# Optimization experiments

Measured on AMD Instinct MI355X. Metric: run time of the kernel, lower is better.

## Reference

```python
import jax, jax.numpy as jnp
import numpy as np

DIM = 1536
NHEADS = 24
HEAD_DIM = DIM // NHEADS
EPS = 1e-6


def rms_norm(x):
    # normalize over last dim, no learned weight
    ms = jnp.mean(x * x, axis=-1, keepdims=True)
    return x * jax.lax.rsqrt(ms + EPS)


def rope_non_neox(x, cos, sin):
    # x: [B, S, H, D]; cos/sin: [S, D] -> broadcast [1, S, 1, D]
    # non-neox (GPT-J / interleaved) style: pairs are (x0,x1),(x2,x3),...
    c = cos[None, :, None, :]
    s = sin[None, :, None, :]
    x1 = x[..., 0::2]
    x2 = x[..., 1::2]
    c1 = c[..., 0::2]
    s1 = s[..., 0::2]
    o1 = x1 * c1 - x2 * s1
    o2 = x2 * c1 + x1 * s1
    out = jnp.stack([o1, o2], axis=-1).reshape(x.shape)
    return out


def setup_inputs() -> dict:
    key = jax.random.key(0)
    k1, k2, k3, k4, k5 = jax.random.split(key, 5)
    B, S = 4, 4096
    x = jax.random.normal(k1, (B, S, DIM), dtype=jnp.float32)
    # rotary tables: build valid cos/sin from random angles (interleaved duplication)
    half = HEAD_DIM // 2
    inv_freq = 1.0 / (10000.0 ** (jnp.arange(0, half, dtype=jnp.float32) / half))
    t = jnp.arange(S, dtype=jnp.float32)
    freqs = jnp.outer(t, inv_freq)  # [S, D/2]
    cos = jnp.repeat(jnp.cos(freqs), 2, axis=-1)  # [S, D] interleaved
    sin = jnp.repeat(jnp.sin(freqs), 2, axis=-1)
    w_qkv = jax.random.normal(k2, (DIM, 3 * DIM), dtype=jnp.float32) * (DIM ** -0.5)
    b_qkv = jax.random.normal(k3, (3 * DIM,), dtype=jnp.float32) * 0.02
    return {"x": x, "cos": cos, "sin": sin, "w_qkv": w_qkv, "b_qkv": b_qkv}


def reference(x, cos, sin, w_qkv, b_qkv):
    B, S, _ = x.shape
    H, D = NHEADS, HEAD_DIM
    qkv = jnp.einsum('bsd,de->bse', x, w_qkv) + b_qkv  # [B,S,3*DIM]
    q, k, v = jnp.split(qkv, 3, axis=-1)
    q = q.reshape(B, S, H, D)
    k = k.reshape(B, S, H, D)
    v = v.reshape(B, S, H, D)
    q = rms_norm(q)
    k = rms_norm(k)
    q = rope_non_neox(q, cos, sin)
    k = rope_non_neox(k, cos, sin)
    # SDPA: [B,H,S,D]
    qh = q.transpose(0, 2, 1, 3)
    kh = k.transpose(0, 2, 1, 3)
    vh = v.transpose(0, 2, 1, 3)
    scale = D ** -0.5
    scores = jnp.einsum('bhqd,bhkd->bhqk', qh, kh) * scale
    attn = jax.nn.softmax(scores, axis=-1)
    out = jnp.einsum('bhqk,bhkd->bhqd', attn, vh)
    out = out.transpose(0, 2, 1, 3).reshape(B, S, H * D)
    return out
```

## Files before the change

### kernel.cpp

```cpp
#include <hip/hip_runtime.h>

#define DIM   1536
#define NQKV  4608
#define NH    24
#define HD    64
#define BATCH 4
#define SEQ   4096
#define ROWS  16384

typedef _Float16 f16x8 __attribute__((ext_vector_type(8)));
typedef float    f32x4 __attribute__((ext_vector_type(4)));

__device__ __forceinline__ void gload_lds16(const void* g, void* l) {
  __builtin_amdgcn_global_load_lds(
      (const __attribute__((address_space(1))) unsigned int*)g,
      (__attribute__((address_space(3))) unsigned int*)l, 16, 0, 0);
}
__device__ __forceinline__ float fexp2(float x) {
#if __has_builtin(__builtin_amdgcn_exp2f)
  return __builtin_amdgcn_exp2f(x);
#else
  return exp2f(x);
#endif
}

#define QSCALE 0.18033688011112042f

__global__ __launch_bounds__(256) void convert_x(const float* __restrict__ X,
                                                 _Float16* __restrict__ Xh) {
  const int i = (blockIdx.x * 256 + threadIdx.x) * 8;
  float4 a = *(const float4*)(X + i);
  float4 b = *(const float4*)(X + i + 4);
  f16x8 h;
  h[0] = (_Float16)a.x; h[1] = (_Float16)a.y; h[2] = (_Float16)a.z; h[3] = (_Float16)a.w;
  h[4] = (_Float16)b.x; h[5] = (_Float16)b.y; h[6] = (_Float16)b.z; h[7] = (_Float16)b.w;
  *(f16x8*)(Xh + i) = h;
}

__global__ __launch_bounds__(256) void transpose_w(const float* __restrict__ W,
                                                   _Float16* __restrict__ Wt) {
  __shared__ float tile[32][33];
  const int tx = threadIdx.x, ty = threadIdx.y;
  const int k0 = blockIdx.y * 32, n0 = blockIdx.x * 32;
  #pragma unroll
  for (int i = 0; i < 32; i += 8)
    tile[ty + i][tx] = W[(size_t)(k0 + ty + i) * NQKV + n0 + tx];
  __syncthreads();
  #pragma unroll
  for (int i = 0; i < 32; i += 8)
    Wt[(size_t)(n0 + ty + i) * DIM + k0 + tx] = (_Float16)tile[tx][ty + i];
}

__global__ __launch_bounds__(256) void qkv_gemm(const _Float16* __restrict__ Xh,
                                                const _Float16* __restrict__ Wt,
                                                const float* __restrict__ Bias,
                                                _Float16* __restrict__ QKV) {
  __shared__ _Float16 As[128 * 64];
  __shared__ _Float16 Bs[128 * 64];
  const int w    = threadIdx.x >> 6;
  const int lane = threadIdx.x & 63;
  const int lr   = lane >> 3, lc = lane & 7;
  const int quad = lane >> 4, l15 = lane & 15;
  const int m0 = blockIdx.y * 128;
  const int n0 = blockIdx.x * 128;
  const int waveR = (w >> 1) * 64;
  const int waveC = (w & 1) * 64;

  f32x4 acc[4][4];
  #pragma unroll
  for (int i = 0; i < 4; i++)
    #pragma unroll
    for (int j = 0; j < 4; j++) acc[i][j] = (f32x4){0.f, 0.f, 0.f, 0.f};

  for (int kt = 0; kt < DIM / 64; ++kt) {
    const int k0 = kt * 64;
    #pragma unroll
    for (int i = 0; i < 4; ++i) {
      const int rr = w * 32 + i * 8;
      gload_lds16(Xh + (size_t)(m0 + rr + lr) * DIM + k0 + lc * 8, &As[rr * 64]);
      gload_lds16(Wt + (size_t)(n0 + rr + lr) * DIM + k0 + lc * 8, &Bs[rr * 64]);
    }
    __syncthreads();
    #pragma unroll
    for (int ks = 0; ks < 2; ++ks) {
      f16x8 aF[4], bF[4];
      #pragma unroll
      for (int t = 0; t < 4; t++)
        aF[t] = *(const f16x8*)&As[(waveR + t * 16 + l15) * 64 + ks * 32 + quad * 8];
      #pragma unroll
      for (int t = 0; t < 4; t++)
        bF[t] = *(const f16x8*)&Bs[(waveC + t * 16 + l15) * 64 + ks * 32 + quad * 8];
      #pragma unroll
      for (int mt = 0; mt < 4; mt++)
        #pragma unroll
        for (int nt = 0; nt < 4; nt++)
          acc[mt][nt] = __builtin_amdgcn_mfma_f32_16x16x32_f16(aF[mt], bF[nt], acc[mt][nt], 0, 0, 0);
    }
    __syncthreads();
  }
  #pragma unroll
  for (int nt = 0; nt < 4; nt++) {
    const int n = n0 + waveC + nt * 16 + l15;
    const float bias = Bias[n];
    #pragma unroll
    for (int mt = 0; mt < 4; mt++) {
      const int mBase = m0 + waveR + mt * 16 + quad * 4;
      #pragma unroll
      for (int r = 0; r < 4; r++)
        QKV[(size_t)(mBase + r) * NQKV + n] = (_Float16)(acc[mt][nt][r] + bias);
    }
  }
}

__global__ __launch_bounds__(256) void rms_rope(_Float16* __restrict__ QKV,
                                                const float* __restrict__ Cos,
                                                const float* __restrict__ Sin) {
  const int gw   = blockIdx.x * 4 + (threadIdx.x >> 6);
  const int lane = threadIdx.x & 63;
  const int row  = gw / NH;
  const int h    = gw - row * NH;
  const int s    = row & (SEQ - 1);

  _Float16* p = QKV + (size_t)row * NQKV + h * HD;
  float q = (float)p[lane];
  float k = (float)p[DIM + lane];

  float sq = q * q, sk = k * k;
  #pragma unroll
  for (int off = 1; off < 64; off <<= 1) {
    sq += __shfl_xor(sq, off);
    sk += __shfl_xor(sk, off);
  }
  q *= rsqrtf(sq * (1.f / 64.f) + 1e-6f);
  k *= rsqrtf(sk * (1.f / 64.f) + 1e-6f);

  const float c  = Cos[s * HD + lane];
  const float si = Sin[s * HD + lane];
  const float qp = __shfl_xor(q, 1);
  const float kp = __shfl_xor(k, 1);
  float oq, ok;
  if (lane & 1) { oq = q * c + qp * si; ok = k * c + kp * si; }
  else          { oq = q * c - qp * si; ok = k * c - kp * si; }

  p[lane]       = (_Float16)(oq * QSCALE);
  p[DIM + lane] = (_Float16)ok;
}

#define LSTR 72
__global__ __launch_bounds__(256) void flash_attn(const _Float16* __restrict__ QKV,
                                                  float* __restrict__ Out) {
  __shared__ __align__(16) _Float16 sm[2 * 64 * LSTR + 4 * 32 * LSTR];
  _Float16* Ks  = sm;
  _Float16* Vts = sm + 64 * LSTR;
  const int w = threadIdx.x >> 6;
  _Float16* Ps = sm + 2 * 64 * LSTR + w * 32 * LSTR;
  const int lane = threadIdx.x & 63;
  const int quad = lane >> 4, l15 = lane & 15;
  const int bh = blockIdx.y;
  const int qt = blockIdx.x;
  const int b  = bh / NH;
  const int h  = bh - b * NH;
  const size_t rowb = (size_t)b * SEQ * NQKV + (size_t)h * HD;

  f16x8 qreg[2][2];
  #pragma unroll
  for (int mt = 0; mt < 2; mt++)
    #pragma unroll
    for (int ks = 0; ks < 2; ks++) {
      const int row = qt * 128 + w * 32 + mt * 16 + l15;
      qreg[mt][ks] = *(const f16x8*)(QKV + rowb + (size_t)row * NQKV + ks * 32 + quad * 8);
    }

  f16x8 onesF;
  {
    const _Float16 one = (_Float16)(l15 == 0 ? 1.0f : 0.0f);
    #pragma unroll
    for (int j = 0; j < 8; j++) onesF[j] = one;
  }

  f32x4 o[2][4], o4[2];
  #pragma unroll
  for (int mt = 0; mt < 2; mt++) {
    o4[mt] = (f32x4){0.f, 0.f, 0.f, 0.f};
    #pragma unroll
    for (int t = 0; t < 4; t++) o[mt][t] = (f32x4){0.f, 0.f, 0.f, 0.f};
  }

  for (int kt = 0; kt < SEQ / 64; ++kt) {
    __syncthreads();
    #pragma unroll
    for (int i = 0; i < 2; i++) {
      const int chunk = threadIdx.x + i * 256;
      const int r = chunk >> 3, c0 = (chunk & 7) * 8;
      *(uint4*)&Ks[r * LSTR + c0] =
          *(const uint4*)(QKV + rowb + (size_t)(kt * 64 + r) * NQKV + DIM + c0);
    }
    #pragma unroll
    for (int i = 0; i < 2; i++) {
      const int c0 = w * 16 + i * 8;
      union { uint4 v; _Float16 u[8]; } d;
      d.v = *(const uint4*)(QKV + rowb + (size_t)(kt * 64 + lane) * NQKV + 2 * DIM + c0);
      #pragma unroll
      for (int j = 0; j < 8; j++) Vts[(c0 + j) * LSTR + lane] = d.u[j];
    }
    __syncthreads();

    f32x4 sacc[2][4];
    #pragma unroll
    for (int mt = 0; mt < 2; mt++)
      #pragma unroll
      for (int t = 0; t < 4; t++) sacc[mt][t] = (f32x4){0.f, 0.f, 0.f, 0.f};
    #pragma unroll
    for (int ks = 0; ks < 2; ks++) {
      f16x8 bF[4];
      #pragma unroll
      for (int t = 0; t < 4; t++)
        bF[t] = *(const f16x8*)&Ks[(t * 16 + l15) * LSTR + ks * 32 + quad * 8];
      #pragma unroll
      for (int mt = 0; mt < 2; mt++)
        #pragma unroll
        for (int t = 0; t < 4; t++)
          sacc[mt][t] = __builtin_amdgcn_mfma_f32_16x16x32_f16(qreg[mt][ks], bF[t], sacc[mt][t], 0, 0, 0);
    }

    #pragma unroll
    for (int mt = 0; mt < 2; mt++)
      #pragma unroll
      for (int t = 0; t < 4; t++)
        #pragma unroll
        for (int r = 0; r < 4; r++) {
          const _Float16 ph = (_Float16)fexp2(sacc[mt][t][r]);
          Ps[(mt * 16 + quad * 4 + r) * LSTR + t * 16 + l15] = ph;
        }

    #pragma unroll
    for (int ks = 0; ks < 2; ks++) {
      f16x8 pF[2];
      #pragma unroll
      for (int mt = 0; mt < 2; mt++)
        pF[mt] = *(const f16x8*)&Ps[(mt * 16 + l15) * LSTR + ks * 32 + quad * 8];
      #pragma unroll
      for (int t = 0; t < 4; t++) {
        f16x8 vF = *(const f16x8*)&Vts[(t * 16 + l15) * LSTR + ks * 32 + quad * 8];
        #pragma unroll
        for (int mt = 0; mt < 2; mt++)
          o[mt][t] = __builtin_amdgcn_mfma_f32_16x16x32_f16(pF[mt], vF, o[mt][t], 0, 0, 0);
      }
      #pragma unroll
      for (int mt = 0; mt < 2; mt++)
        o4[mt] = __builtin_amdgcn_mfma_f32_16x16x32_f16(pF[mt], onesF, o4[mt], 0, 0, 0);
    }
  }

  #pragma unroll
  for (int mt = 0; mt < 2; mt++) {
    float lrow[4];
    #pragma unroll
    for (int r = 0; r < 4; r++) lrow[r] = __shfl(o4[mt][r], lane & 48);
    #pragma unroll
    for (int t = 0; t < 4; t++)
      #pragma unroll
      for (int r = 0; r < 4; r++) {
        const int srow = qt * 128 + w * 32 + mt * 16 + quad * 4 + r;
        const int d = t * 16 + l15;
        Out[((size_t)(b * SEQ + srow)) * DIM + h * HD + d] = o[mt][t][r] / lrow[r];
      }
  }
}

extern "C" void kernel_launch(void* const* d_in, const int* in_sizes, int n_in,
                              void* d_out, int out_size, void* d_ws, size_t ws_size,
                              hipStream_t stream) {
  const float* X    = (const float*)d_in[0];
  const float* Cos  = (const float*)d_in[1];
  const float* Sin  = (const float*)d_in[2];
  const float* W    = (const float*)d_in[3];
  const float* Bias = (const float*)d_in[4];
  float* Out = (float*)d_out;

  char* ws = (char*)d_ws;
  _Float16* Xh  = (_Float16*)(ws);
  _Float16* Wt  = (_Float16*)(ws + 50331648);
  _Float16* QKV = (_Float16*)(ws + 64487424);

  convert_x  <<<dim3(ROWS * DIM / (8 * 256)), 256, 0, stream>>>(X, Xh);
  transpose_w<<<dim3(NQKV / 32, DIM / 32), dim3(32, 8), 0, stream>>>(W, Wt);
  qkv_gemm   <<<dim3(NQKV / 128, ROWS / 128), 256, 0, stream>>>(Xh, Wt, Bias, QKV);
  rms_rope   <<<dim3(ROWS * NH / 4), 256, 0, stream>>>(QKV, Cos, Sin);
  flash_attn <<<dim3(SEQ / 128, BATCH * NH), 256, 0, stream>>>(QKV, Out);
}
```

Before: 1.275 ms.

## Fuse RMSNorm and RoPE into QKV GEMM epilogue; swizzle attention block order

Removes the separate rms_rope kernel and applies the per-head RMS normalization, interleaved rotary embedding and Q scaling directly in the GEMM epilogue, where each wave's 64 columns line up with one head. This avoids a full extra read and write of the Q/K portion of the QKV buffer and one kernel launch. The flash attention grid becomes 1D with a swizzled block index that spreads consecutive blocks across heads, likely aimed at XCD/L2 locality. The epilogue now does extra shuffles and reads cos/sin per element, which may add register pressure to the GEMM.

Result: slower. 1.318 ms (+3.3%).

```diff
diff --git a/kernel.cpp b/kernel.cpp
--- a/kernel.cpp
+++ b/kernel.cpp
@@ -54,6 +54,8 @@
 __global__ __launch_bounds__(256) void qkv_gemm(const _Float16* __restrict__ Xh,
                                                 const _Float16* __restrict__ Wt,
                                                 const float* __restrict__ Bias,
+                                                const float* __restrict__ Cos,
+                                                const float* __restrict__ Sin,
                                                 _Float16* __restrict__ QKV) {
   __shared__ _Float16 As[128 * 64];
   __shared__ _Float16 Bs[128 * 64];
@@ -98,55 +100,63 @@
     }
     __syncthreads();
   }
-  #pragma unroll
-  for (int nt = 0; nt < 4; nt++) {
-    const int n = n0 + waveC + nt * 16 + l15;
-    const float bias = Bias[n];
+
+  const int nCol0  = n0 + waveC;
+  const int region = nCol0 / DIM;
+
+  float bias[4];
+  #pragma unroll
+  for (int nt = 0; nt < 4; nt++) bias[nt] = Bias[nCol0 + nt * 16 + l15];
+
+  if (region == 2) {
+    #pragma unroll
+    for (int nt = 0; nt < 4; nt++) {
+      const int n = nCol0 + nt * 16 + l15;
+      #pragma unroll
+      for (int mt = 0; mt < 4; mt++) {
+        const int mBase = m0 + waveR + mt * 16 + quad * 4;
+        #pragma unroll
+        for (int r = 0; r < 4; r++)
+          QKV[(size_t)(mBase + r) * NQKV + n] = (_Float16)(acc[mt][nt][r] + bias[nt]);
+      }
+    }
+  } else {
+    const float qsc = (region == 0) ? QSCALE : 1.0f;
     #pragma unroll
     for (int mt = 0; mt < 4; mt++) {
       const int mBase = m0 + waveR + mt * 16 + quad * 4;
       #pragma unroll
-      for (int r = 0; r < 4; r++)
-        QKV[(size_t)(mBase + r) * NQKV + n] = (_Float16)(acc[mt][nt][r] + bias);
-    }
-  }
-}
-
-__global__ __launch_bounds__(256) void rms_rope(_Float16* __restrict__ QKV,
-                                                const float* __restrict__ Cos,
-                                                const float* __restrict__ Sin) {
-  const int gw   = blockIdx.x * 4 + (threadIdx.x >> 6);
-  const int lane = threadIdx.x & 63;
-  const int row  = gw / NH;
-  const int h    = gw - row * NH;
-  const int s    = row & (SEQ - 1);
-
-  _Float16* p = QKV + (size_t)row * NQKV + h * HD;
-  float q = (float)p[lane];
-  float k = (float)p[DIM + lane];
-
-  float sq = q * q, sk = k * k;
-  #pragma unroll
-  for (int off = 1; off < 64; off <<= 1) {
-    sq += __shfl_xor(sq, off);
-    sk += __shfl_xor(sk, off);
-  }
-  q *= rsqrtf(sq * (1.f / 64.f) + 1e-6f);
-  k *= rsqrtf(sk * (1.f / 64.f) + 1e-6f);
-
-  const float c  = Cos[s * HD + lane];
-  const float si = Sin[s * HD + lane];
-  const float qp = __shfl_xor(q, 1);
-  const float kp = __shfl_xor(k, 1);
-  float oq, ok;
-  if (lane & 1) { oq = q * c + qp * si; ok = k * c + kp * si; }
-  else          { oq = q * c - qp * si; ok = k * c - kp * si; }
-
-  p[lane]       = (_Float16)(oq * QSCALE);
-  p[DIM + lane] = (_Float16)ok;
+      for (int r = 0; r < 4; r++) {
+        const int m = mBase + r;
+        const int s = m & (SEQ - 1);
+        float v[4];
+        float ss = 0.f;
+        #pragma unroll
+        for (int nt = 0; nt < 4; nt++) {
+          v[nt] = acc[mt][nt][r] + bias[nt];
+          ss += v[nt] * v[nt];
+        }
+        #pragma unroll
+        for (int off = 1; off < 16; off <<= 1) ss += __shfl_xor(ss, off);
+        const float rinv = rsqrtf(ss * (1.f / 64.f) + 1e-6f);
+        #pragma unroll
+        for (int nt = 0; nt < 4; nt++) {
+          const int d = nt * 16 + l15;
+          const float c  = Cos[s * HD + d];
+          const float si = Sin[s * HD + d];
+          const float x  = v[nt] * rinv;
+          const float xp = __shfl_xor(x, 1);
+          float o = (l15 & 1) ? (x * c + xp * si) : (x * c - xp * si);
+          o *= qsc;
+          QKV[(size_t)m * NQKV + nCol0 + d] = (_Float16)o;
+        }
+      }
+    }
+  }
 }
 
 #define LSTR 72
+#define NBLK (SEQ / 128 * BATCH * NH)
 __global__ __launch_bounds__(256) void flash_attn(const _Float16* __restrict__ QKV,
                                                   float* __restrict__ Out) {
   __shared__ __align__(16) _Float16 sm[2 * 64 * LSTR + 4 * 32 * LSTR];
@@ -156,8 +166,10 @@
   _Float16* Ps = sm + 2 * 64 * LSTR + w * 32 * LSTR;
   const int lane = threadIdx.x & 63;
   const int quad = lane >> 4, l15 = lane & 15;
-  const int bh = blockIdx.y;
-  const int qt = blockIdx.x;
+  const int Lraw = blockIdx.x;
+  const int swz  = (Lraw & 7) * (NBLK / 8) + (Lraw >> 3);
+  const int qt = swz & 31;
+  const int bh = swz >> 5;
   const int b  = bh / NH;
   const int h  = bh - b * NH;
   const size_t rowb = (size_t)b * SEQ * NQKV + (size_t)h * HD;
@@ -285,7 +297,6 @@
 
   convert_x  <<<dim3(ROWS * DIM / (8 * 256)), 256, 0, stream>>>(X, Xh);
   transpose_w<<<dim3(NQKV / 32, DIM / 32), dim3(32, 8), 0, stream>>>(W, Wt);
-  qkv_gemm   <<<dim3(NQKV / 128, ROWS / 128), 256, 0, stream>>>(Xh, Wt, Bias, QKV);
-  rms_rope   <<<dim3(ROWS * NH / 4), 256, 0, stream>>>(QKV, Cos, Sin);
-  flash_attn <<<dim3(SEQ / 128, BATCH * NH), 256, 0, stream>>>(QKV, Out);
-}
+  qkv_gemm   <<<dim3(NQKV / 128, ROWS / 128), 256, 0, stream>>>(Xh, Wt, Bias, Cos, Sin, QKV);
+  flash_attn <<<dim3(NBLK), 256, 0, stream>>>(QKV, Out);
+}
```
